# Performance work log

Hardware: AMD Instinct MI355X
Metric: run time of the kernel (lower is better)

The kernel has to match this reference:

```python
import jax, jax.numpy as jnp
import numpy as np


def setup_inputs() -> dict:
    key = jax.random.key(0)
    inputs = jax.random.normal(key, (8, 4096, 512), dtype=jnp.float32)
    return {"inputs": inputs}


def reference(inputs) -> jnp.ndarray:
    # Faithful math: out = (X @ X^T) @ X  per batch.
    # Expressed via the associativity-equivalent X @ (X^T @ X), which computes
    # the identical result while avoiding the O(S^2) intermediate (S >> D).
    gram = jnp.einsum('bsd,bse->bde', inputs, inputs)   # [B, D, D]
    out = jnp.einsum('bsd,bde->bse', inputs, gram)      # [B, S, D]
    return out
```

## Files before the change

### kernel.cpp

```cpp
#include <hip/hip_runtime.h>
#include <hip/hip_bf16.h>


typedef __attribute__((ext_vector_type(8))) short short8;
typedef __attribute__((ext_vector_type(4))) float floatx4;

#define BM 128
#define BN 128
#define BK 32

#define BATCH 8
#define SEQ 4096
#define DIM 512

__device__ __forceinline__ void async_copy16(const __hip_bfloat16* g, __hip_bfloat16* l) {
  __builtin_amdgcn_global_load_lds((const __attribute__((address_space(1))) void*)g,
                                   (__attribute__((address_space(3))) void*)l, 16, 0, 0);
}

__global__ __launch_bounds__(256) void transpose_cast_kernel(
    const float* __restrict__ X, __hip_bfloat16* __restrict__ Xt,
    __hip_bfloat16* __restrict__ Xb16) {
  __shared__ float tile[64][65];
  const int b = blockIdx.z;
  const int s0 = blockIdx.x * 64;
  const int d0 = blockIdx.y * 64;
  const int tid = threadIdx.x;
  const int tx = tid & 63;
  const int ty = tid >> 6;
  const float* Xb = X + (long)b * SEQ * DIM;
  __hip_bfloat16* Xtb = Xt + (long)b * DIM * SEQ;
#pragma unroll
  for (int r = 0; r < 64; r += 4)
    tile[r + ty][tx] = Xb[(long)(s0 + r + ty) * DIM + d0 + tx];
  __syncthreads();
#pragma unroll
  for (int it = 0; it < 2; ++it) {
    const int idx = it * 256 + tid;
    const int dl = idx >> 3;
    const int so = (idx & 7) * 8;
    union { short8 v; __hip_bfloat16 e[8]; } u;
#pragma unroll
    for (int j = 0; j < 8; ++j) u.e[j] = __float2bfloat16(tile[so + j][dl]);
    *(short8*)&Xtb[(long)(d0 + dl) * SEQ + s0 + so] = u.v;
  }
  if (Xb16 != nullptr) {
    __hip_bfloat16* Xcb = Xb16 + (long)b * SEQ * DIM;
#pragma unroll
    for (int it = 0; it < 2; ++it) {
      const int idx = it * 256 + tid;
      const int sl = idx >> 3;
      const int dc = idx & 7;
      union { short8 v; __hip_bfloat16 e[8]; } u;
#pragma unroll
      for (int j = 0; j < 8; ++j) u.e[j] = __float2bfloat16(tile[sl][dc * 8 + j]);
      *(short8*)&Xcb[(long)(s0 + sl) * DIM + d0 + dc * 8] = u.v;
    }
  }
}

template <int NSPLIT, bool AFP32, int SWZ>
__global__ __launch_bounds__(256) void gemm_bt_kernel(
    const float* __restrict__ Af, const __hip_bfloat16* __restrict__ Ab,
    const __hip_bfloat16* __restrict__ Bt, float* __restrict__ C,
    int K, int lda, int ldb, int ldc, long strideA, long strideB, long strideC) {
  __shared__ __align__(16) __hip_bfloat16 As[BM * BK];
  __shared__ __align__(16) __hip_bfloat16 Bs[BN * BK];

  int bz, m0, n0;
  if constexpr (SWZ == 1) {
    const int lin = blockIdx.x;
    bz = blockIdx.z;
    const int xcd = lin & 7;
    const int t = lin >> 3;
    n0 = (t & 3) * BN;
    m0 = ((t >> 2) * 8 + xcd) * BM;
  } else if constexpr (SWZ == 2) {
    bz = blockIdx.x;
    const int t = blockIdx.y;
    m0 = (t >> 2) * BM;
    n0 = (t & 3) * BN;
  } else {
    bz = blockIdx.z;
    m0 = blockIdx.y * BM;
    n0 = blockIdx.x * BN;
  }
  const int b = bz / NSPLIT;
  const int split = bz % NSPLIT;
  const int klen = K / NSPLIT;
  const int kb = split * klen;

  const int tid = threadIdx.x;
  const int w = tid >> 6;
  const int lane = tid & 63;
  const int r16 = lane & 15;
  const int kg = lane >> 4;
  const int wr = w >> 1;
  const int wc = w & 1;

  const float* Afb = AFP32 ? Af + b * strideA : nullptr;
  const __hip_bfloat16* Abb = AFP32 ? nullptr : Ab + b * strideA;
  const __hip_bfloat16* Btb = Bt + b * strideB;
  float* Cb = C + (long)bz * strideC;

  const floatx4 vzero = {0.f, 0.f, 0.f, 0.f};
  floatx4 acc[4][4];
#pragma unroll
  for (int i = 0; i < 4; ++i)
#pragma unroll
    for (int j = 0; j < 4; ++j) acc[i][j] = vzero;

  const int arow = tid >> 1;
  const int ahalf = tid & 1;
  float f[16];
  if constexpr (AFP32) {
    const float* ar = Afb + (long)(m0 + arow) * lda + kb + ahalf * 16;
    *(float4*)(f + 0)  = *(const float4*)(ar + 0);
    *(float4*)(f + 4)  = *(const float4*)(ar + 4);
    *(float4*)(f + 8)  = *(const float4*)(ar + 8);
    *(float4*)(f + 12) = *(const float4*)(ar + 12);
  }

  for (int k0 = kb; k0 < kb + klen; k0 += BK) {
#pragma unroll
    for (int q = 0; q < 2; ++q) {
      const __hip_bfloat16* gb =
          Btb + (long)(n0 + w * 32 + q * 16 + (lane >> 2)) * ldb + k0 + (lane & 3) * 8;
      async_copy16(gb, &Bs[(w * 32 + q * 16) * BK]);
    }
    if constexpr (!AFP32) {
#pragma unroll
      for (int q = 0; q < 2; ++q) {
        const __hip_bfloat16* ga =
            Abb + (long)(m0 + w * 32 + q * 16 + (lane >> 2)) * lda + k0 + (lane & 3) * 8;
        async_copy16(ga, &As[(w * 32 + q * 16) * BK]);
      }
    } else {
      union { short8 v[2]; __hip_bfloat16 e[16]; } u;
#pragma unroll
      for (int t = 0; t < 16; ++t) u.e[t] = __float2bfloat16(f[t]);
      short8* dst = (short8*)&As[arow * BK + ahalf * 16];
      dst[0] = u.v[0];
      dst[1] = u.v[1];
    }
    __syncthreads();

    if constexpr (AFP32) {
      if (k0 + BK < kb + klen) {
        const float* ar = Afb + (long)(m0 + arow) * lda + (k0 + BK) + ahalf * 16;
        *(float4*)(f + 0)  = *(const float4*)(ar + 0);
        *(float4*)(f + 4)  = *(const float4*)(ar + 4);
        *(float4*)(f + 8)  = *(const float4*)(ar + 8);
        *(float4*)(f + 12) = *(const float4*)(ar + 12);
      }
    }

    short8 a[4], bfrag[4];
#pragma unroll
    for (int i = 0; i < 4; ++i)
      a[i] = *(const short8*)&As[(wr * 64 + i * 16 + r16) * BK + kg * 8];
#pragma unroll
    for (int j = 0; j < 4; ++j)
      bfrag[j] = *(const short8*)&Bs[(wc * 64 + j * 16 + r16) * BK + kg * 8];
#pragma unroll
    for (int i = 0; i < 4; ++i)
#pragma unroll
      for (int j = 0; j < 4; ++j)
        acc[i][j] = __builtin_amdgcn_mfma_f32_16x16x32_bf16(a[i], bfrag[j], acc[i][j], 0, 0, 0);
    __syncthreads();
  }

#pragma unroll
  for (int i = 0; i < 4; ++i) {
    const int row_base = m0 + wr * 64 + i * 16 + kg * 4;
#pragma unroll
    for (int j = 0; j < 4; ++j) {
      const int col = n0 + wc * 64 + j * 16 + r16;
#pragma unroll
      for (int r = 0; r < 4; ++r)
        Cb[(long)(row_base + r) * ldc + col] = acc[i][j][r];
    }
  }
}

template <int NSPLIT>
__global__ __launch_bounds__(256) void reduce_cast_kernel(
    const float* __restrict__ P, __hip_bfloat16* __restrict__ G) {
  const int DD4 = DIM * DIM / 4;
  const long idx = (long)blockIdx.x * 256 + threadIdx.x;
  const int b = (int)(idx / DD4);
  const int e = (int)(idx % DD4);
  const float4* base = (const float4*)P + (long)(b * NSPLIT) * DD4 + e;
  float4 s = base[0];
#pragma unroll
  for (int p = 1; p < NSPLIT; ++p) {
    float4 t = base[(long)p * DD4];
    s.x += t.x; s.y += t.y; s.z += t.z; s.w += t.w;
  }
  union { short s4[4]; uint2 v; } u;
  u.s4[0] = __bfloat16_as_short(__float2bfloat16(s.x));
  u.s4[1] = __bfloat16_as_short(__float2bfloat16(s.y));
  u.s4[2] = __bfloat16_as_short(__float2bfloat16(s.z));
  u.s4[3] = __bfloat16_as_short(__float2bfloat16(s.w));
  *(uint2*)&G[idx * 4] = u.v;
}

extern "C" void kernel_launch(void* const* d_in, const int* in_sizes, int n_in,
                              void* d_out, int out_size, void* d_ws, size_t ws_size,
                              hipStream_t stream) {
  const float* X = (const float*)d_in[0];
  float* out = (float*)d_out;
  const long xtBytes = (long)BATCH * DIM * SEQ * 2;
  const long gramBytes = (long)BATCH * DIM * DIM * 2;
  const long part8Bytes = (long)BATCH * 8 * DIM * DIM * 4;
  __hip_bfloat16* Xt = (__hip_bfloat16*)d_out;
  __hip_bfloat16* gram = (__hip_bfloat16*)d_ws;

  const bool bigWs = ws_size >= (size_t)(gramBytes + xtBytes + part8Bytes);
  const bool midWs = ws_size >= (size_t)(gramBytes + xtBytes);
  __hip_bfloat16* Xb16 = midWs ? (__hip_bfloat16*)((char*)d_ws + gramBytes) : nullptr;

  transpose_cast_kernel<<<dim3(SEQ / 64, DIM / 64, BATCH), 256, 0, stream>>>(X, Xt, Xb16);

  if (bigWs) {
    float* partials = (float*)((char*)d_ws + gramBytes + xtBytes);
    gemm_bt_kernel<8, false, 2><<<dim3(BATCH * 8, 16, 1), 256, 0, stream>>>(
        nullptr, Xt, Xt, partials, SEQ, SEQ, SEQ, DIM,
        (long)DIM * SEQ, (long)DIM * SEQ, (long)DIM * DIM);
    reduce_cast_kernel<8><<<dim3(BATCH * DIM * DIM / 4 / 256), 256, 0, stream>>>(
        partials, gram);
  } else {
    float* partials = (float*)((char*)d_out + xtBytes);
    gemm_bt_kernel<4, false, 2><<<dim3(BATCH * 4, 16, 1), 256, 0, stream>>>(
        nullptr, Xt, Xt, partials, SEQ, SEQ, SEQ, DIM,
        (long)DIM * SEQ, (long)DIM * SEQ, (long)DIM * DIM);
    reduce_cast_kernel<4><<<dim3(BATCH * DIM * DIM / 4 / 256), 256, 0, stream>>>(
        partials, gram);
  }

  if (midWs) {
    gemm_bt_kernel<1, false, 1><<<dim3(128, 1, BATCH), 256, 0, stream>>>(
        nullptr, Xb16, gram, out, DIM, DIM, DIM, DIM,
        (long)SEQ * DIM, (long)DIM * DIM, (long)SEQ * DIM);
  } else {
    gemm_bt_kernel<1, true, 1><<<dim3(128, 1, BATCH), 256, 0, stream>>>(
        X, nullptr, gram, out, DIM, DIM, DIM, DIM,
        (long)SEQ * DIM, (long)DIM * DIM, (long)SEQ * DIM);
  }
}
```

Measured before the change: 196.8 us.

## Double-buffer GEMM LDS tiles and use split-K of four for the gram

Adds double-buffered shared memory to the bf16 GEMM so the async global-to-LDS loads for the next K tile are issued before the MFMA work on the current tile. This removes one barrier per iteration and overlaps load latency with compute. The gram GEMM also always uses a split-K of four, which halves the partial-sum traffic and reduction work but launches half as many blocks (512 instead of 1024). LDS use doubles per block, which may lower occupancy.

```diff
diff --git a/kernel.cpp b/kernel.cpp
--- a/kernel.cpp
+++ b/kernel.cpp
@@ -64,8 +64,8 @@
     const float* __restrict__ Af, const __hip_bfloat16* __restrict__ Ab,
     const __hip_bfloat16* __restrict__ Bt, float* __restrict__ C,
     int K, int lda, int ldb, int ldc, long strideA, long strideB, long strideC) {
-  __shared__ __align__(16) __hip_bfloat16 As[BM * BK];
-  __shared__ __align__(16) __hip_bfloat16 Bs[BN * BK];
+  __shared__ __align__(16) __hip_bfloat16 As[2][BM * BK];
+  __shared__ __align__(16) __hip_bfloat16 Bs[2][BN * BK];
 
   int bz, m0, n0;
   if constexpr (SWZ == 1) {
@@ -113,61 +113,74 @@
   const int arow = tid >> 1;
   const int ahalf = tid & 1;
   float f[16];
-  if constexpr (AFP32) {
-    const float* ar = Afb + (long)(m0 + arow) * lda + kb + ahalf * 16;
+
+  auto stageB = [&](int buf, int k0) {
+#pragma unroll
+    for (int q = 0; q < 2; ++q) {
+      const __hip_bfloat16* gb =
+          Btb + (long)(n0 + w * 32 + q * 16 + (lane >> 2)) * ldb + k0 + (lane & 3) * 8;
+      async_copy16(gb, &Bs[buf][(w * 32 + q * 16) * BK]);
+    }
+  };
+  auto stageA = [&](int buf, int k0) {
+#pragma unroll
+    for (int q = 0; q < 2; ++q) {
+      const __hip_bfloat16* ga =
+          Abb + (long)(m0 + w * 32 + q * 16 + (lane >> 2)) * lda + k0 + (lane & 3) * 8;
+      async_copy16(ga, &As[buf][(w * 32 + q * 16) * BK]);
+    }
+  };
+  auto loadF = [&](int k0) {
+    const float* ar = Afb + (long)(m0 + arow) * lda + k0 + ahalf * 16;
     *(float4*)(f + 0)  = *(const float4*)(ar + 0);
     *(float4*)(f + 4)  = *(const float4*)(ar + 4);
     *(float4*)(f + 8)  = *(const float4*)(ar + 8);
     *(float4*)(f + 12) = *(const float4*)(ar + 12);
-  }
-
-  for (int k0 = kb; k0 < kb + klen; k0 += BK) {
-#pragma unroll
-    for (int q = 0; q < 2; ++q) {
-      const __hip_bfloat16* gb =
-          Btb + (long)(n0 + w * 32 + q * 16 + (lane >> 2)) * ldb + k0 + (lane & 3) * 8;
-      async_copy16(gb, &Bs[(w * 32 + q * 16) * BK]);
-    }
-    if constexpr (!AFP32) {
-#pragma unroll
-      for (int q = 0; q < 2; ++q) {
-        const __hip_bfloat16* ga =
-            Abb + (long)(m0 + w * 32 + q * 16 + (lane >> 2)) * lda + k0 + (lane & 3) * 8;
-        async_copy16(ga, &As[(w * 32 + q * 16) * BK]);
+  };
+  auto writeF = [&](int buf) {
+    union { short8 v[2]; __hip_bfloat16 e[16]; } u;
+#pragma unroll
+    for (int t = 0; t < 16; ++t) u.e[t] = __float2bfloat16(f[t]);
+    short8* dst = (short8*)&As[buf][arow * BK + ahalf * 16];
+    dst[0] = u.v[0];
+    dst[1] = u.v[1];
+  };
+
+  const int nIter = klen / BK;
+  if constexpr (AFP32) {
+    loadF(kb);
+    writeF(0);
+    loadF(kb + BK);
+  } else {
+    stageA(0, kb);
+  }
+  stageB(0, kb);
+
+  for (int t = 0; t < nIter; ++t) {
+    const int cur = t & 1;
+    __syncthreads();
+    if (t + 1 < nIter) {
+      if constexpr (AFP32) {
+        writeF(cur ^ 1);
+        if (t + 2 < nIter) loadF(kb + (t + 2) * BK);
+      } else {
+        stageA(cur ^ 1, kb + (t + 1) * BK);
       }
-    } else {
-      union { short8 v[2]; __hip_bfloat16 e[16]; } u;
-#pragma unroll
-      for (int t = 0; t < 16; ++t) u.e[t] = __float2bfloat16(f[t]);
-      short8* dst = (short8*)&As[arow * BK + ahalf * 16];
-      dst[0] = u.v[0];
-      dst[1] = u.v[1];
-    }
-    __syncthreads();
-
-    if constexpr (AFP32) {
-      if (k0 + BK < kb + klen) {
-        const float* ar = Afb + (long)(m0 + arow) * lda + (k0 + BK) + ahalf * 16;
-        *(float4*)(f + 0)  = *(const float4*)(ar + 0);
-        *(float4*)(f + 4)  = *(const float4*)(ar + 4);
-        *(float4*)(f + 8)  = *(const float4*)(ar + 8);
-        *(float4*)(f + 12) = *(const float4*)(ar + 12);
-      }
+      stageB(cur ^ 1, kb + (t + 1) * BK);
     }
 
     short8 a[4], bfrag[4];
 #pragma unroll
     for (int i = 0; i < 4; ++i)
-      a[i] = *(const short8*)&As[(wr * 64 + i * 16 + r16) * BK + kg * 8];
+      a[i] = *(const short8*)&As[cur][(wr * 64 + i * 16 + r16) * BK + kg * 8];
 #pragma unroll
     for (int j = 0; j < 4; ++j)
-      bfrag[j] = *(const short8*)&Bs[(wc * 64 + j * 16 + r16) * BK + kg * 8];
+      bfrag[j] = *(const short8*)&Bs[cur][(wc * 64 + j * 16 + r16) * BK + kg * 8];
 #pragma unroll
     for (int i = 0; i < 4; ++i)
 #pragma unroll
       for (int j = 0; j < 4; ++j)
         acc[i][j] = __builtin_amdgcn_mfma_f32_16x16x32_bf16(a[i], bfrag[j], acc[i][j], 0, 0, 0);
-    __syncthreads();
   }
 
 #pragma unroll
@@ -212,31 +225,23 @@
   float* out = (float*)d_out;
   const long xtBytes = (long)BATCH * DIM * SEQ * 2;
   const long gramBytes = (long)BATCH * DIM * DIM * 2;
-  const long part8Bytes = (long)BATCH * 8 * DIM * DIM * 4;
+  const long part4Bytes = (long)BATCH * 4 * DIM * DIM * 4;
   __hip_bfloat16* Xt = (__hip_bfloat16*)d_out;
   __hip_bfloat16* gram = (__hip_bfloat16*)d_ws;
 
-  const bool bigWs = ws_size >= (size_t)(gramBytes + xtBytes + part8Bytes);
+  const bool bigWs = ws_size >= (size_t)(gramBytes + xtBytes + part4Bytes);
   const bool midWs = ws_size >= (size_t)(gramBytes + xtBytes);
   __hip_bfloat16* Xb16 = midWs ? (__hip_bfloat16*)((char*)d_ws + gramBytes) : nullptr;
 
   transpose_cast_kernel<<<dim3(SEQ / 64, DIM / 64, BATCH), 256, 0, stream>>>(X, Xt, Xb16);
 
-  if (bigWs) {
-    float* partials = (float*)((char*)d_ws + gramBytes + xtBytes);
-    gemm_bt_kernel<8, false, 2><<<dim3(BATCH * 8, 16, 1), 256, 0, stream>>>(
-        nullptr, Xt, Xt, partials, SEQ, SEQ, SEQ, DIM,
-        (long)DIM * SEQ, (long)DIM * SEQ, (long)DIM * DIM);
-    reduce_cast_kernel<8><<<dim3(BATCH * DIM * DIM / 4 / 256), 256, 0, stream>>>(
-        partials, gram);
-  } else {
-    float* partials = (float*)((char*)d_out + xtBytes);
-    gemm_bt_kernel<4, false, 2><<<dim3(BATCH * 4, 16, 1), 256, 0, stream>>>(
-        nullptr, Xt, Xt, partials, SEQ, SEQ, SEQ, DIM,
-        (long)DIM * SEQ, (long)DIM * SEQ, (long)DIM * DIM);
-    reduce_cast_kernel<4><<<dim3(BATCH * DIM * DIM / 4 / 256), 256, 0, stream>>>(
-        partials, gram);
-  }
+  float* partials = bigWs ? (float*)((char*)d_ws + gramBytes + xtBytes)
+                          : (float*)((char*)d_out + xtBytes);
+  gemm_bt_kernel<4, false, 2><<<dim3(BATCH * 4, 16, 1), 256, 0, stream>>>(
+      nullptr, Xt, Xt, partials, SEQ, SEQ, SEQ, DIM,
+      (long)DIM * SEQ, (long)DIM * SEQ, (long)DIM * DIM);
+  reduce_cast_kernel<4><<<dim3(BATCH * DIM * DIM / 4 / 256), 256, 0, stream>>>(
+      partials, gram);
 
   if (midWs) {
     gemm_bt_kernel<1, false, 1><<<dim3(128, 1, BATCH), 256, 0, stream>>>(
```

Measured after the change: 172.0 us. -12.6%, faster.
